# Optimization experiments

Measured on AMD Instinct MI355X. Metric: run time of the kernel, lower is better.

The kernel has to match this reference:

```python
import jax, jax.numpy as jnp
import numpy as np

N_STEPS = 2
S_MAX = 3.0
BUDGET = 32.0

def _unit(x):
    n = jnp.linalg.norm(x, axis=-1, keepdims=True)
    return x / jnp.maximum(n, 1e-12)

def setup_inputs() -> dict:
    key = jax.random.key(0)
    ks = jax.random.split(key, 12)
    BS, B, M, D, N = 8, 4, 2048, 128, 1024
    seed = jax.random.normal(ks[0], (BS, N, D), jnp.float32)
    w_cand = jax.random.normal(ks[1], (BS, N, D), jnp.float32)
    novelty = jax.random.uniform(ks[2], (BS, N), jnp.float32)
    g_em = jax.random.uniform(ks[3], (BS,), jnp.float32)
    em_K = _unit(jax.random.normal(ks[4], (BS, B, M, D), jnp.float32))
    em_V = jax.random.normal(ks[5], (BS, B, M, D), jnp.float32)
    em_S = jax.random.uniform(ks[6], (BS, B, M), jnp.float32)
    em_age = jax.random.uniform(ks[7], (BS, B, M), jnp.float32)
    w1 = jax.random.normal(ks[8], (B, D), jnp.float32) * 0.02
    w2 = jax.random.normal(ks[9], (B, D), jnp.float32) * 0.02
    gate_bias = jnp.zeros((B, D), jnp.float32)
    raw_tau = jnp.zeros((B,), jnp.float32)
    raw_tau_w = jnp.zeros((B,), jnp.float32)
    return dict(seed=seed, w_cand=w_cand, novelty=novelty, g_em=g_em,
                em_K=em_K, em_V=em_V, em_S=em_S, em_age=em_age,
                w1=w1, w2=w2, gate_bias=gate_bias,
                raw_tau=raw_tau, raw_tau_w=raw_tau_w, b=0)

def reference(seed, w_cand, novelty, g_em, em_K, em_V, em_S, em_age,
              w1, w2, gate_bias, raw_tau, raw_tau_w, b):
    Kb = em_K[:, b]          # [BS, M, D]
    Vb = em_V[:, b]          # [BS, M, D]
    Sb = em_S[:, b]          # [BS, M]
    ageb = em_age[:, b]      # [BS, M]
    active = (Sb > 0)[:, None, :]  # [BS, 1, M]

    # ---- trail_read (eval mode: no sigma noise) ----
    tau = jax.nn.softplus(raw_tau[b]) + 0.1
    y = seed
    for _ in range(N_STEPS):
        scores = jnp.einsum('bnd,bmd->bnm', y, Kb) / tau
        scores = jnp.where(active, scores, -jnp.inf)
        attn = jnp.nan_to_num(jax.nn.softmax(scores, axis=-1), nan=0.0)
        delta = jnp.einsum('bnm,bmd->bnd', attn, Vb)
        gate = jax.nn.sigmoid(w1[b] * y + w2[b] * delta + gate_bias[b])
        y = y + gate * delta
    y_em = y - seed

    # ---- commit: soft routing -> aggregate -> neuromodulated EMA ----
    tau_w = jax.nn.softplus(raw_tau_w[b]) + 0.1
    M_slots = Kb.shape[1]
    w_norm = _unit(w_cand)
    route_scores = jnp.einsum('bnd,bmd->bnm', w_norm, Kb) / tau_w
    route_scores = jnp.where(active, route_scores, -jnp.inf)
    route = jnp.nan_to_num(jax.nn.softmax(route_scores, axis=-1), nan=1.0 / M_slots)
    weighted_route = novelty[..., None] * route           # [BS, N, M]
    route_agg = weighted_route.mean(axis=1)               # [BS, M]
    denom = jnp.maximum(weighted_route.sum(axis=1), 1e-8)[..., None]  # [BS, M, 1]
    update_K = jnp.einsum('bnm,bnd->bmd', weighted_route, w_norm) / denom
    update_V = jnp.einsum('bnm,bnd->bmd', weighted_route, w_cand) / denom
    alpha = jnp.minimum(g_em[:, None] * route_agg, 1.0)   # [BS, M]
    a = alpha[..., None]
    new_K = (1 - a) * Kb + a * _unit(update_K)
    new_V = (1 - a) * Vb + a * update_V
    new_S = jnp.clip(Sb + alpha, 0.0, S_MAX)
    new_age = ageb * (1 - alpha)
    # budget_enforce: rescale strengths so each row sums to at most BUDGET
    scale = jnp.minimum(1.0, BUDGET / jnp.maximum(new_S.sum(-1, keepdims=True), 1e-8))
    new_S = new_S * scale
    return (y_em, new_K, new_V, new_S, new_age)
```

## Files before the change

kernel.cpp:

```cpp
#include <hip/hip_runtime.h>
#include <hip/hip_bf16.h>
#include <math.h>

#define BS_ 8
#define B_  4
#define M_  2048
#define D_  128
#define N_  1024
#define NEG (-1e30f)

typedef unsigned short us_t;
typedef __attribute__((ext_vector_type(8))) short bf8v;
typedef __attribute__((ext_vector_type(4))) float f4v;

__device__ __forceinline__ float softplus_(float x) {
    return (x > 20.0f) ? x : log1pf(expf(x));
}
__device__ __forceinline__ float dot4_acc(float4 a, float4 b, float acc) {
    acc = fmaf(a.x, b.x, acc);
    acc = fmaf(a.y, b.y, acc);
    acc = fmaf(a.z, b.z, acc);
    acc = fmaf(a.w, b.w, acc);
    return acc;
}
__device__ __forceinline__ us_t f2bf(float x) {
    __hip_bfloat16 h = __float2bfloat16(x);
    return __builtin_bit_cast(us_t, h);
}
__device__ __forceinline__ float bf2f(us_t u) {
    unsigned v = ((unsigned)u) << 16;
    return __builtin_bit_cast(float, v);
}
__device__ __forceinline__ int swz(int us_idx, int row) { return us_idx ^ ((row & 7) << 3); }

__global__ __launch_bounds__(256, 2) void conv_k(
    const float* __restrict__ w_cand, const float* __restrict__ emK,
    const float* __restrict__ emV, const int* __restrict__ bp,
    us_t* __restrict__ Kbf, us_t* __restrict__ Wcg,
    us_t* __restrict__ WcTg, us_t* __restrict__ Vtg, float* __restrict__ invnW)
{
    __shared__ float wt[64][132];
    __shared__ float invn[64];
    const int tid = threadIdx.x;
    const int bs  = blockIdx.y;
    const int bx  = blockIdx.x;
    const int b   = bp[0];

    if (bx < 32) {
        const float* src = emK + ((size_t)(bs * B_ + b)) * M_ * D_ + (size_t)bx * 64 * D_;
        us_t* dst = Kbf + (size_t)bs * M_ * D_ + (size_t)bx * 64 * D_;
        for (int i = tid; i < 64 * 128 / 4; i += 256) {
            float4 v = ((const float4*)src)[i];
            ushort4 o;
            o.x = f2bf(v.x); o.y = f2bf(v.y); o.z = f2bf(v.z); o.w = f2bf(v.w);
            ((ushort4*)dst)[i] = o;
        }
        return;
    }
    if (bx >= 48) {
        const int m0 = (bx - 48) * 64;
        const float* Vb = emV + ((size_t)(bs * B_ + b)) * M_ * D_ + (size_t)m0 * D_;
        for (int c = tid; c < 64 * 32; c += 256) {
            int row = c >> 5, col = (c & 31) << 2;
            *(float4*)&wt[row][col] = *(const float4*)&Vb[row * D_ + col];
        }
        __syncthreads();
        us_t* VtB = Vtg + (size_t)bs * D_ * M_;
        for (int c = tid; c < 1024; c += 256) {
            int d = c >> 3, mc = c & 7;
            uint4 o;
            o.x = (unsigned)f2bf(wt[mc * 8 + 0][d]) | ((unsigned)f2bf(wt[mc * 8 + 1][d]) << 16);
            o.y = (unsigned)f2bf(wt[mc * 8 + 2][d]) | ((unsigned)f2bf(wt[mc * 8 + 3][d]) << 16);
            o.z = (unsigned)f2bf(wt[mc * 8 + 4][d]) | ((unsigned)f2bf(wt[mc * 8 + 5][d]) << 16);
            o.w = (unsigned)f2bf(wt[mc * 8 + 6][d]) | ((unsigned)f2bf(wt[mc * 8 + 7][d]) << 16);
            *(uint4*)&VtB[(size_t)d * M_ + m0 + mc * 8] = o;
        }
        return;
    }
    const int n0 = (bx - 32) * 64;
    const float* Wb = w_cand + (size_t)bs * N_ * D_ + (size_t)n0 * D_;
    for (int c = tid; c < 64 * 32; c += 256) {
        int row = c >> 5, col = (c & 31) << 2;
        *(float4*)&wt[row][col] = *(const float4*)&Wb[row * D_ + col];
    }
    __syncthreads();
    {
        int r = tid >> 2, j = tid & 3;
        float ss = 0.0f;
        #pragma unroll
        for (int q = 0; q < 8; ++q) {
            float4 v = *(float4*)&wt[r][q * 16 + j * 4];
            ss = dot4_acc(v, v, ss);
        }
        ss += __shfl_xor(ss, 1, 4);
        ss += __shfl_xor(ss, 2, 4);
        if (j == 0) invn[r] = 1.0f / fmaxf(sqrtf(ss), 1e-12f);
    }
    __syncthreads();
    us_t* WcB = Wcg + (size_t)bs * N_ * D_ + (size_t)n0 * D_;
    for (int e = tid; e < 8192; e += 256) {
        int row = e >> 7, col = e & 127;
        WcB[row * D_ + col] = f2bf(wt[row][col]);
    }
    us_t* WcTB = WcTg + (size_t)bs * D_ * N_;
    for (int e = tid; e < 8192; e += 256) {
        int d = e >> 6, n = e & 63;
        WcTB[d * N_ + n0 + n] = f2bf(wt[n][d]);
    }
    if (tid < 64) invnW[(size_t)bs * N_ + n0 + tid] = invn[tid];
}

__global__ __launch_bounds__(256, 2) void attn_part_k(
    const float* __restrict__ ySrc, const us_t* __restrict__ Kbf,
    const us_t* __restrict__ Vtg, const float* __restrict__ emS,
    const float* __restrict__ raw_tau, const int* __restrict__ bp,
    us_t* __restrict__ pDelta, float2* __restrict__ pML)
{
    __shared__ us_t KtL[2][8192];
    __shared__ us_t VtL[2][8192];
    __shared__ us_t Pl[4][1024];
    __shared__ float sbt[2][64];

    const int tid = threadIdx.x;
    const int raw = blockIdx.x;
    const int logical = (raw & 7) * 64 + (raw >> 3);
    const int bs = logical >> 6;
    const int rem = logical & 63;
    const int nt = rem >> 2;
    const int q  = rem & 3;
    const int b = bp[0];
    const float rtau = 1.0f / (softplus_(raw_tau[b]) + 0.1f);

    const us_t* KbB = Kbf + (size_t)bs * M_ * D_ + (size_t)(q * 512) * D_;
    const us_t* VtB = Vtg + (size_t)bs * D_ * M_;
    const float* SbB = emS + ((size_t)(bs * B_ + b)) * M_ + q * 512;

    const int wave = tid >> 6, lane = tid & 63;
    const int r = lane & 15, kg = lane >> 4;

    bf8v yb[4];
    {
        const float* yrow = ySrc + ((size_t)bs * N_ + nt * 64 + wave * 16 + r) * D_;
        #pragma unroll
        for (int kk = 0; kk < 4; ++kk) {
            float4 a = *(const float4*)&yrow[kk * 32 + kg * 8];
            float4 c = *(const float4*)&yrow[kk * 32 + kg * 8 + 4];
            bf8v t;
            t[0] = (short)f2bf(a.x); t[1] = (short)f2bf(a.y);
            t[2] = (short)f2bf(a.z); t[3] = (short)f2bf(a.w);
            t[4] = (short)f2bf(c.x); t[5] = (short)f2bf(c.y);
            t[6] = (short)f2bf(c.z); t[7] = (short)f2bf(c.w);
            yb[kk] = t;
        }
    }

    uint4 kr[4], vr[4];
    float sreg = 0.0f;

#define AP_LOAD(t) do {                                                           \
        for (int i = 0; i < 4; ++i) {                                             \
            int c = tid + i * 256;                                                \
            kr[i] = *(const uint4*)&KbB[(size_t)((t) * 64 + (c >> 4)) * D_ + ((c & 15) << 3)]; \
            vr[i] = *(const uint4*)&VtB[(size_t)(c >> 3) * M_ + q * 512 + (t) * 64 + ((c & 7) << 3)]; \
        }                                                                         \
        if (tid < 64) sreg = SbB[(t) * 64 + tid];                                 \
    } while (0)

#define AP_WRITE(bf) do {                                                         \
        for (int i = 0; i < 4; ++i) {                                             \
            int c = tid + i * 256;                                                \
            int ki = (c >> 4) * 128 + ((c & 15) << 3);                            \
            *(uint4*)&KtL[bf][swz(ki, c >> 4)] = kr[i];                           \
            int vi = (c >> 3) * 64 + ((c & 7) << 3);                              \
            *(uint4*)&VtL[bf][swz(vi, c >> 3)] = vr[i];                           \
        }                                                                         \
        if (tid < 64) sbt[bf][tid] = sreg;                                        \
    } while (0)

    f4v cD[8];
    #pragma unroll
    for (int df = 0; df < 8; ++df) cD[df] = (f4v){0.f, 0.f, 0.f, 0.f};
    float mrun = NEG, lsum = 0.0f;

    AP_LOAD(0);
    AP_WRITE(0);
    __syncthreads();

    for (int t = 0; t < 8; ++t) {
        const int cur = t & 1;
        if (t < 7) AP_LOAD(t + 1);

        float sv[4][4];
        #pragma unroll
        for (int mf = 0; mf < 4; ++mf) {
            f4v c4 = {0.f, 0.f, 0.f, 0.f};
            #pragma unroll
            for (int kk = 0; kk < 4; ++kk) {
                int row_ = mf * 16 + r;
                bf8v a = *(bf8v*)&KtL[cur][swz(row_ * 128 + kk * 32 + kg * 8, row_)];
                c4 = __builtin_amdgcn_mfma_f32_16x16x32_bf16(a, yb[kk], c4, 0, 0, 0);
            }
            #pragma unroll
            for (int reg = 0; reg < 4; ++reg) {
                int ml = mf * 16 + kg * 4 + reg;
                sv[mf][reg] = (sbt[cur][ml] > 0.0f) ? c4[reg] * rtau : NEG;
            }
        }
        float tmax = NEG;
        #pragma unroll
        for (int mf = 0; mf < 4; ++mf)
            #pragma unroll
            for (int reg = 0; reg < 4; ++reg) tmax = fmaxf(tmax, sv[mf][reg]);
        tmax = fmaxf(tmax, __shfl_xor(tmax, 16, 64));
        tmax = fmaxf(tmax, __shfl_xor(tmax, 32, 64));
        float mnew = fmaxf(mrun, tmax);
        float f = (mnew > -1e29f) ? __expf(mrun - mnew) : 1.0f;
        mrun = mnew;

        float psum = 0.0f;
        #pragma unroll
        for (int mf = 0; mf < 4; ++mf)
            #pragma unroll
            for (int reg = 0; reg < 4; ++reg) {
                float p = (sv[mf][reg] > -1e29f) ? __expf(sv[mf][reg] - mnew) : 0.0f;
                psum += p;
                int ml = mf * 16 + kg * 4 + reg;
                Pl[wave][swz(r * 64 + ml, r)] = f2bf(p);
            }
        lsum = lsum * f + psum;

        float fr[4];
        #pragma unroll
        for (int reg = 0; reg < 4; ++reg) fr[reg] = __shfl(f, kg * 4 + reg, 64);
        #pragma unroll
        for (int df = 0; df < 8; ++df)
            #pragma unroll
            for (int reg = 0; reg < 4; ++reg) cD[df][reg] *= fr[reg];

        #pragma unroll
        for (int kk = 0; kk < 2; ++kk) {
            bf8v pa = *(bf8v*)&Pl[wave][swz(r * 64 + kk * 32 + kg * 8, r)];
            #pragma unroll
            for (int df = 0; df < 8; ++df) {
                int row_ = df * 16 + r;
                bf8v bv = *(bf8v*)&VtL[cur][swz(row_ * 64 + kk * 32 + kg * 8, row_)];
                cD[df] = __builtin_amdgcn_mfma_f32_16x16x32_bf16(pa, bv, cD[df], 0, 0, 0);
            }
        }

        if (t < 7) AP_WRITE(cur ^ 1);
        __syncthreads();
    }
#undef AP_LOAD
#undef AP_WRITE

    lsum += __shfl_xor(lsum, 16, 64);
    lsum += __shfl_xor(lsum, 32, 64);
    float invl = (lsum > 0.0f) ? 1.0f / lsum : 0.0f;

    us_t* pd = pDelta + ((size_t)((bs * 16 + nt) * 4 + q)) * (64 * 128);
    #pragma unroll
    for (int reg = 0; reg < 4; ++reg) {
        float il = __shfl(invl, kg * 4 + reg, 64);
        int nrow = wave * 16 + kg * 4 + reg;
        #pragma unroll
        for (int df = 0; df < 8; ++df)
            pd[nrow * 128 + df * 16 + r] = f2bf(cD[df][reg] * il);
    }
    if (kg == 0) {
        int nrow = wave * 16 + r;
        pML[((size_t)((bs * 16 + nt) * 4 + q)) * 64 + nrow] = make_float2(mrun, lsum);
    }
}

__global__ __launch_bounds__(256, 2) void attn_merge_k(
    const float* __restrict__ ySrc, const float* __restrict__ seed,
    const us_t* __restrict__ pDelta, const float2* __restrict__ pML,
    const float* __restrict__ w1, const float* __restrict__ w2,
    const float* __restrict__ gb, const int* __restrict__ bp,
    float* __restrict__ yOut, int mode)
{
    __shared__ float w1L[128], w2L[128], gbL[128];
    const int tid = threadIdx.x, raw = blockIdx.x;
    const int logical = (raw & 7) * 16 + (raw >> 3);
    const int bs = logical >> 4, nt = logical & 15;
    const int b = bp[0];
    if (tid < 128) {
        w1L[tid] = w1[b * D_ + tid];
        w2L[tid] = w2[b * D_ + tid];
        gbL[tid] = gb[b * D_ + tid];
    }
    __syncthreads();
    const int rw = tid >> 2, dj = tid & 3;
    const size_t base = ((size_t)(bs * 16 + nt)) * 4;
    float2 ml0 = pML[(base + 0) * 64 + rw];
    float2 ml1 = pML[(base + 1) * 64 + rw];
    float2 ml2 = pML[(base + 2) * 64 + rw];
    float2 ml3 = pML[(base + 3) * 64 + rw];
    float M = fmaxf(fmaxf(ml0.x, ml1.x), fmaxf(ml2.x, ml3.x));
    float w0 = 0.f, wA = 0.f, wB = 0.f, w3 = 0.f, tot = 0.f;
    if (M > -1e29f) {
        w0 = ml0.y * __expf(ml0.x - M);
        wA = ml1.y * __expf(ml1.x - M);
        wB = ml2.y * __expf(ml2.x - M);
        w3 = ml3.y * __expf(ml3.x - M);
        tot = w0 + wA + wB + w3;
    }
    float inv = (tot > 0.0f) ? 1.0f / tot : 0.0f;
    w0 *= inv; wA *= inv; wB *= inv; w3 *= inv;

    const us_t* pd0 = pDelta + (base + 0) * 8192 + rw * 128;
    const us_t* pd1 = pDelta + (base + 1) * 8192 + rw * 128;
    const us_t* pd2 = pDelta + (base + 2) * 8192 + rw * 128;
    const us_t* pd3 = pDelta + (base + 3) * 8192 + rw * 128;
    const float* yrow = ySrc + ((size_t)bs * N_ + nt * 64 + rw) * D_;
    const float* srow = seed + ((size_t)bs * N_ + nt * 64 + rw) * D_;
    float* orow = yOut + ((size_t)bs * N_ + nt * 64 + rw) * D_;

    #pragma unroll
    for (int e = 0; e < 4; ++e) {
        int d0 = dj * 32 + e * 8;
        uint4 u0 = *(const uint4*)&pd0[d0];
        uint4 u1 = *(const uint4*)&pd1[d0];
        uint4 u2 = *(const uint4*)&pd2[d0];
        uint4 u3 = *(const uint4*)&pd3[d0];
        const us_t* a0 = (const us_t*)&u0;
        const us_t* a1 = (const us_t*)&u1;
        const us_t* a2 = (const us_t*)&u2;
        const us_t* a3 = (const us_t*)&u3;
        float4 ya = *(const float4*)&yrow[d0];
        float4 yc = *(const float4*)&yrow[d0 + 4];
        float yv[8] = {ya.x, ya.y, ya.z, ya.w, yc.x, yc.y, yc.z, yc.w};
        float res[8];
        #pragma unroll
        for (int j = 0; j < 8; ++j) {
            float dl = w0 * bf2f(a0[j]) + wA * bf2f(a1[j]) + wB * bf2f(a2[j]) + w3 * bf2f(a3[j]);
            int d = d0 + j;
            float g = 1.0f / (1.0f + __expf(-(w1L[d] * yv[j] + w2L[d] * dl + gbL[d])));
            res[j] = yv[j] + g * dl;
        }
        if (mode == 1) {
            float4 sa = *(const float4*)&srow[d0];
            float4 sc = *(const float4*)&srow[d0 + 4];
            res[0] -= sa.x; res[1] -= sa.y; res[2] -= sa.z; res[3] -= sa.w;
            res[4] -= sc.x; res[5] -= sc.y; res[6] -= sc.z; res[7] -= sc.w;
        }
        float4 o1; o1.x = res[0]; o1.y = res[1]; o1.z = res[2]; o1.w = res[3];
        float4 o2; o2.x = res[4]; o2.y = res[5]; o2.z = res[6]; o2.w = res[7];
        *(float4*)&orow[d0] = o1;
        *(float4*)&orow[d0 + 4] = o2;
    }
}

__global__ __launch_bounds__(256, 2) void stats_k(
    const us_t* __restrict__ Wcg, const us_t* __restrict__ Kbf,
    const float* __restrict__ invnW, const float* __restrict__ emS,
    const float* __restrict__ raw_tau_w, const int* __restrict__ bp,
    float* __restrict__ mxW, float* __restrict__ smW)
{
    __shared__ us_t KtL[2][8192];
    __shared__ float sbt[2][64];

    const int tid = threadIdx.x;
    const int raw = blockIdx.x;
    const int logical = (raw & 7) * 64 + (raw >> 3);
    const int bs = logical >> 6;
    const int rem = logical & 63;
    const int nt = rem >> 2;
    const int q  = rem & 3;
    const int b = bp[0];
    const float rtw = 1.0f / (softplus_(raw_tau_w[b]) + 0.1f);

    const us_t* KbB = Kbf + (size_t)bs * M_ * D_ + (size_t)(q * 512) * D_;
    const float* SbB = emS + ((size_t)(bs * B_ + b)) * M_ + q * 512;

    const int wave = tid >> 6, lane = tid & 63;
    const int r = lane & 15, kg = lane >> 4;
    const int n = nt * 64 + wave * 16 + r;

    bf8v wb[4];
    {
        const us_t* wrow = Wcg + ((size_t)bs * N_ + n) * D_;
        #pragma unroll
        for (int kk = 0; kk < 4; ++kk)
            wb[kk] = *(const bf8v*)&wrow[kk * 32 + kg * 8];
    }
    const float ivn = invnW[(size_t)bs * N_ + n];

    uint4 kr[4];
    float sreg = 0.0f;

#define ST_LOAD(t) do {                                                           \
        for (int i = 0; i < 4; ++i) {                                             \
            int c = tid + i * 256;                                                \
            kr[i] = *(const uint4*)&KbB[(size_t)((t) * 64 + (c >> 4)) * D_ + ((c & 15) << 3)]; \
        }                                                                         \
        if (tid < 64) sreg = SbB[(t) * 64 + tid];                                 \
    } while (0)

#define ST_WRITE(bf) do {                                                         \
        for (int i = 0; i < 4; ++i) {                                             \
            int c = tid + i * 256;                                                \
            int ki = (c >> 4) * 128 + ((c & 15) << 3);                            \
            *(uint4*)&KtL[bf][swz(ki, c >> 4)] = kr[i];                           \
        }                                                                         \
        if (tid < 64) sbt[bf][tid] = sreg;                                        \
    } while (0)

    float mx = NEG, sm = 0.0f;

    ST_LOAD(0);
    ST_WRITE(0);
    __syncthreads();

    for (int t = 0; t < 8; ++t) {
        const int cur = t & 1;
        if (t < 7) ST_LOAD(t + 1);

        #pragma unroll
        for (int mf = 0; mf < 4; ++mf) {
            f4v c4 = {0.f, 0.f, 0.f, 0.f};
            #pragma unroll
            for (int kk = 0; kk < 4; ++kk) {
                int row_ = mf * 16 + r;
                bf8v a = *(bf8v*)&KtL[cur][swz(row_ * 128 + kk * 32 + kg * 8, row_)];
                c4 = __builtin_amdgcn_mfma_f32_16x16x32_bf16(a, wb[kk], c4, 0, 0, 0);
            }
            float v[4]; bool act[4];
            float lm = NEG;
            #pragma unroll
            for (int reg = 0; reg < 4; ++reg) {
                int ml = mf * 16 + kg * 4 + reg;
                v[reg] = c4[reg] * ivn * rtw;
                act[reg] = (sbt[cur][ml] > 0.0f);
                if (act[reg]) lm = fmaxf(lm, v[reg]);
            }
            float mnew = fmaxf(mx, lm);
            if (mnew > -1e29f) {
                float acc = sm * __expf(mx - mnew);
                #pragma unroll
                for (int reg = 0; reg < 4; ++reg)
                    if (act[reg]) acc += __expf(v[reg] - mnew);
                sm = acc; mx = mnew;
            }
        }

        if (t < 7) ST_WRITE(cur ^ 1);
        __syncthreads();
    }
#undef ST_LOAD
#undef ST_WRITE

    #pragma unroll
    for (int off = 16; off <= 32; off <<= 1) {
        float omx = __shfl_xor(mx, off, 64);
        float osm = __shfl_xor(sm, off, 64);
        float nm = fmaxf(mx, omx);
        if (nm > -1e29f) sm = sm * __expf(mx - nm) + osm * __expf(omx - nm);
        else sm = 0.0f;
        mx = nm;
    }
    if (kg == 0) {
        mxW[(size_t)(q * BS_ + bs) * N_ + n] = mx;
        smW[(size_t)(q * BS_ + bs) * N_ + n] = sm;
    }
}

__global__ __launch_bounds__(256) void stats_fin_k(
    const float* __restrict__ mxW, const float* __restrict__ smW,
    const float* __restrict__ novelty,
    float* __restrict__ mxF, float* __restrict__ rivF, float* __restrict__ punF)
{
    int idx = blockIdx.x * 256 + threadIdx.x;
    float m[4], s[4];
    #pragma unroll
    for (int q = 0; q < 4; ++q) {
        m[q] = mxW[q * (BS_ * N_) + idx];
        s[q] = smW[q * (BS_ * N_) + idx];
    }
    float MX = fmaxf(fmaxf(m[0], m[1]), fmaxf(m[2], m[3]));
    float SM = 0.0f;
    if (MX > -1e29f) {
        #pragma unroll
        for (int q = 0; q < 4; ++q)
            if (m[q] > -1e29f) SM += s[q] * __expf(m[q] - MX);
    }
    float nov = novelty[idx];
    if (SM > 0.0f) { mxF[idx] = MX; rivF[idx] = nov / SM; punF[idx] = -1.0f; }
    else           { mxF[idx] = 0.0f; rivF[idx] = 0.0f; punF[idx] = nov * (1.0f / (float)M_); }
}

__global__ __launch_bounds__(256) void update2_k(
    const us_t* __restrict__ Kbf, const us_t* __restrict__ Wcg,
    const us_t* __restrict__ WcTg, const float* __restrict__ g_em,
    const float* __restrict__ emK, const float* __restrict__ emV,
    const float* __restrict__ emS, const float* __restrict__ emAge,
    const float* __restrict__ raw_tau_w, const int* __restrict__ bp,
    const float* __restrict__ invnW, const float* __restrict__ mxF,
    const float* __restrict__ rivF, const float* __restrict__ punF,
    float* __restrict__ outK, float* __restrict__ outV,
    float* __restrict__ outS, float* __restrict__ outA)
{
    __shared__ us_t KaL[8192];
    __shared__ us_t WcL[2][8192];
    __shared__ us_t WcTL[2][8192];
    __shared__ us_t Pl[4096];
    __shared__ us_t P2l[4096];
    __shared__ float4 cns[2][64];
    __shared__ float sbL[64], csL[64], alphaL[64];

    const int tid = threadIdx.x;
    const int raw = blockIdx.x;
    const int logical = (raw & 7) * 32 + (raw >> 3);
    const int bs = logical >> 5;
    const int m0 = (logical & 31) * 64;
    const int b = bp[0];
    const float rtw = 1.0f / (softplus_(raw_tau_w[b]) + 0.1f);
    const float ge = g_em[bs];

    const us_t* KaG = Kbf + (size_t)bs * M_ * D_ + (size_t)m0 * D_;
    const us_t* WcB = Wcg + (size_t)bs * N_ * D_;
    const us_t* WcTB = WcTg + (size_t)bs * D_ * N_;

    for (int c = tid; c < 64 * 16; c += 256) {
        int row = c >> 4, off = (c & 15) << 3;
        uint4 v = *(const uint4*)&KaG[row * 128 + off];
        *(uint4*)&KaL[swz(row * 128 + off, row)] = v;
    }
    if (tid < 64) sbL[tid] = emS[((size_t)(bs * B_ + b)) * M_ + m0 + tid];
    __syncthreads();

    const int wave = tid >> 6, lane = tid & 63;
    const int r = lane & 15, kg = lane >> 4;
    const int mf = wave;

    bf8v a_s[4];
    #pragma unroll
    for (int kk = 0; kk < 4; ++kk) {
        int row = mf * 16 + r;
        a_s[kk] = *(bf8v*)&KaL[swz(row * 128 + kk * 32 + kg * 8, row)];
    }
    bool act4[4];
    #pragma unroll
    for (int reg = 0; reg < 4; ++reg) act4[reg] = (sbL[mf * 16 + kg * 4 + reg] > 0.0f);

    f4v cK[8], cV[8];
    #pragma unroll
    for (int df = 0; df < 8; ++df) { cK[df] = (f4v){0,0,0,0}; cV[df] = (f4v){0,0,0,0}; }
    float csp[4] = {0.f, 0.f, 0.f, 0.f};

    uint4 wr[4], wtr[4];
    float4 creg = {0.f, 0.f, 0.f, 0.f};

#define UP_LOAD(t) do {                                                            \
        for (int i = 0; i < 4; ++i) {                                              \
            int c = tid + i * 256;                                                 \
            wr[i]  = *(const uint4*)&WcB[((size_t)((t) * 64 + (c >> 4))) * D_ + ((c & 15) << 3)]; \
            wtr[i] = *(const uint4*)&WcTB[((size_t)(c >> 3)) * N_ + (t) * 64 + ((c & 7) << 3)];   \
        }                                                                          \
        if (tid < 64) {                                                            \
            int nn = (t) * 64 + tid;                                               \
            creg.x = mxF[(size_t)bs * N_ + nn];                                    \
            creg.y = rivF[(size_t)bs * N_ + nn];                                   \
            creg.z = punF[(size_t)bs * N_ + nn];                                   \
            creg.w = invnW[(size_t)bs * N_ + nn];                                  \
        }                                                                          \
    } while (0)

#define UP_WRITE(bf) do {                                                          \
        for (int i = 0; i < 4; ++i) {                                              \
            int c = tid + i * 256;                                                 \
            int ki = (c >> 4) * 128 + ((c & 15) << 3);                             \
            *(uint4*)&WcL[bf][swz(ki, c >> 4)] = wr[i];                            \
            int vi = (c >> 3) * 64 + ((c & 7) << 3);                               \
            *(uint4*)&WcTL[bf][swz(vi, c >> 3)] = wtr[i];                          \
        }                                                                          \
        if (tid < 64) cns[bf][tid] = creg;                                         \
    } while (0)

    UP_LOAD(0);
    UP_WRITE(0);
    __syncthreads();

    for (int nt = 0; nt < 16; ++nt) {
        const int cur = nt & 1;
        if (nt < 15) UP_LOAD(nt + 1);

        #pragma unroll
        for (int nf = 0; nf < 4; ++nf) {
            f4v c = {0.f, 0.f, 0.f, 0.f};
            #pragma unroll
            for (int kk = 0; kk < 4; ++kk) {
                int row = nf * 16 + r;
                bf8v bb = *(bf8v*)&WcL[cur][swz(row * 128 + kk * 32 + kg * 8, row)];
                c = __builtin_amdgcn_mfma_f32_16x16x32_bf16(a_s[kk], bb, c, 0, 0, 0);
            }
            int nl = nf * 16 + r;
            float4 cn = cns[cur][nl];
            #pragma unroll
            for (int reg = 0; reg < 4; ++reg) {
                float p;
                if (cn.z >= 0.0f) p = cn.z;
                else p = act4[reg] ? cn.y * __expf(c[reg] * cn.w * rtw - cn.x) : 0.0f;
                csp[reg] += p;
                int mrow = mf * 16 + kg * 4 + reg;
                Pl[swz(mrow * 64 + nl, mrow)] = f2bf(p);
                P2l[swz(mrow * 64 + nl, mrow)] = f2bf(p * cn.w);
            }
        }
        #pragma unroll
        for (int kk2 = 0; kk2 < 2; ++kk2) {
            int prow = mf * 16 + r;
            bf8v pa  = *(bf8v*)&Pl[swz(prow * 64 + kk2 * 32 + kg * 8, prow)];
            bf8v pa2 = *(bf8v*)&P2l[swz(prow * 64 + kk2 * 32 + kg * 8, prow)];
            #pragma unroll
            for (int df = 0; df < 8; ++df) {
                int row = df * 16 + r;
                bf8v bw = *(bf8v*)&WcTL[cur][swz(row * 64 + kk2 * 32 + kg * 8, row)];
                cV[df] = __builtin_amdgcn_mfma_f32_16x16x32_bf16(pa, bw, cV[df], 0, 0, 0);
                cK[df] = __builtin_amdgcn_mfma_f32_16x16x32_bf16(pa2, bw, cK[df], 0, 0, 0);
            }
        }

        if (nt < 15) UP_WRITE(cur ^ 1);
        __syncthreads();
    }
#undef UP_LOAD
#undef UP_WRITE

    #pragma unroll
    for (int reg = 0; reg < 4; ++reg) {
        float v = csp[reg];
        v += __shfl_xor(v, 1, 16);
        v += __shfl_xor(v, 2, 16);
        v += __shfl_xor(v, 4, 16);
        v += __shfl_xor(v, 8, 16);
        csp[reg] = v;
    }
    if (r == 0) {
        #pragma unroll
        for (int reg = 0; reg < 4; ++reg) csL[mf * 16 + kg * 4 + reg] = csp[reg];
    }
    __syncthreads();
    if (tid < 64) alphaL[tid] = fminf(ge * csL[tid] * (1.0f / (float)N_), 1.0f);
    __syncthreads();

    float rden[4], nrm[4];
    #pragma unroll
    for (int reg = 0; reg < 4; ++reg) {
        int ml = mf * 16 + kg * 4 + reg;
        rden[reg] = 1.0f / fmaxf(csL[ml], 1e-8f);
        float s = 0.0f;
        #pragma unroll
        for (int df = 0; df < 8; ++df) {
            float u = cK[df][reg] * rden[reg];
            s += u * u;
        }
        s += __shfl_xor(s, 1, 16);
        s += __shfl_xor(s, 2, 16);
        s += __shfl_xor(s, 4, 16);
        s += __shfl_xor(s, 8, 16);
        nrm[reg] = 1.0f / fmaxf(sqrtf(s), 1e-12f);
    }

    const float* KbG = emK + ((size_t)(bs * B_ + b)) * M_ * D_ + (size_t)m0 * D_;
    const float* VbG = emV + ((size_t)(bs * B_ + b)) * M_ * D_ + (size_t)m0 * D_;
    float* oK = outK + (size_t)bs * M_ * D_ + (size_t)m0 * D_;
    float* oV = outV + (size_t)bs * M_ * D_ + (size_t)m0 * D_;
    #pragma unroll
    for (int reg = 0; reg < 4; ++reg) {
        int ml = mf * 16 + kg * 4 + reg;
        float a = alphaL[ml];
        #pragma unroll
        for (int df = 0; df < 8; ++df) {
            int d = df * 16 + r;
            float uK = cK[df][reg] * rden[reg] * nrm[reg];
            float uV = cV[df][reg] * rden[reg];
            oK[ml * D_ + d] = (1.0f - a) * KbG[ml * D_ + d] + a * uK;
            oV[ml * D_ + d] = (1.0f - a) * VbG[ml * D_ + d] + a * uV;
        }
    }
    if (tid < 64) {
        float a = alphaL[tid];
        float sp = fminf(fmaxf(sbL[tid] + a, 0.0f), 3.0f);
        outS[(size_t)bs * M_ + m0 + tid] = sp;
        outA[(size_t)bs * M_ + m0 + tid] =
            emAge[((size_t)(bs * B_ + b)) * M_ + m0 + tid] * (1.0f - a);
    }
}

__global__ __launch_bounds__(256) void scale_s_k(float* __restrict__ outS)
{
    __shared__ float wsum[4];
    const int bs = blockIdx.x, tid = threadIdx.x;
    float* p = outS + (size_t)bs * M_;
    float s = 0.0f;
    for (int i = tid; i < M_; i += 256) s += p[i];
    #pragma unroll
    for (int o = 32; o >= 1; o >>= 1) s += __shfl_xor(s, o, 64);
    if ((tid & 63) == 0) wsum[tid >> 6] = s;
    __syncthreads();
    float tot = wsum[0] + wsum[1] + wsum[2] + wsum[3];
    float scale = fminf(1.0f, 32.0f / fmaxf(tot, 1e-8f));
    for (int i = tid; i < M_; i += 256) p[i] *= scale;
}

extern "C" void kernel_launch(void* const* d_in, const int* in_sizes, int n_in,
                              void* d_out, int out_size, void* d_ws, size_t ws_size,
                              hipStream_t stream) {
    (void)in_sizes; (void)n_in; (void)out_size; (void)ws_size;
    const float* seed    = (const float*)d_in[0];
    const float* w_cand  = (const float*)d_in[1];
    const float* novelty = (const float*)d_in[2];
    const float* g_em    = (const float*)d_in[3];
    const float* emK     = (const float*)d_in[4];
    const float* emV     = (const float*)d_in[5];
    const float* emS     = (const float*)d_in[6];
    const float* emAge   = (const float*)d_in[7];
    const float* w1      = (const float*)d_in[8];
    const float* w2      = (const float*)d_in[9];
    const float* gb      = (const float*)d_in[10];
    const float* rt      = (const float*)d_in[11];
    const float* rtw     = (const float*)d_in[12];
    const int*   bp      = (const int*)d_in[13];

    float* out  = (float*)d_out;
    float* yem  = out;
    float* outK = out + 1048576;
    float* outV = out + 3145728;
    float* outS = out + 5242880;
    float* outA = out + 5259264;

    us_t* Kbf = (us_t*)d_ws;
    us_t* Wcg = Kbf + (size_t)BS_ * M_ * D_;
    us_t* WcT = Wcg + (size_t)BS_ * N_ * D_;
    us_t* Vtg = WcT + (size_t)BS_ * D_ * N_;
    us_t* pDelta = Vtg + (size_t)BS_ * D_ * M_;
    float* fb   = (float*)(pDelta + (size_t)512 * 64 * 128);
    float* invnW = fb;
    float* mxW   = invnW + BS_ * N_;
    float* smW   = mxW + 4 * BS_ * N_;
    float* mxF   = smW + 4 * BS_ * N_;
    float* rivF  = mxF + BS_ * N_;
    float* punF  = rivF + BS_ * N_;
    float* y1    = punF + BS_ * N_;
    float2* pML  = (float2*)(y1 + (size_t)BS_ * N_ * D_);

    conv_k<<<dim3(80, 8), 256, 0, stream>>>(w_cand, emK, emV, bp, Kbf, Wcg, WcT, Vtg, invnW);

    attn_part_k<<<dim3(512), 256, 0, stream>>>(seed, Kbf, Vtg, emS, rt, bp, pDelta, pML);
    attn_merge_k<<<dim3(128), 256, 0, stream>>>(seed, seed, pDelta, pML, w1, w2, gb, bp, y1, 0);
    attn_part_k<<<dim3(512), 256, 0, stream>>>(y1, Kbf, Vtg, emS, rt, bp, pDelta, pML);
    attn_merge_k<<<dim3(128), 256, 0, stream>>>(y1, seed, pDelta, pML, w1, w2, gb, bp, yem, 1);

    stats_k<<<dim3(512), 256, 0, stream>>>(Wcg, Kbf, invnW, emS, rtw, bp, mxW, smW);
    stats_fin_k<<<dim3(32), 256, 0, stream>>>(mxW, smW, novelty, mxF, rivF, punF);
    update2_k<<<dim3(256), 256, 0, stream>>>(Kbf, Wcg, WcT, g_em, emK, emV, emS, emAge,
                                             rtw, bp, invnW, mxF, rivF, punF,
                                             outK, outV, outS, outA);
    scale_s_k<<<8, 256, 0, stream>>>(outS);
}
```

Baseline: 268.2 us.

## Split update kernel into 32-row tiles with N-split waves and LDS reduction

The commit update kernel now processes 32 memory slots per block instead of 64, launching 512 blocks instead of 256. Within each block, the four waves split as two M-fragments times two N-halves, and partial K/V accumulators are reduced through shared memory at the end. The double-buffered LDS staging is replaced by a single buffer with register prefetch, and the K fragments are loaded straight from global memory. This aims to raise occupancy and parallelism on the many-CU GPU, at the cost of extra syncs per tile, an extra reduction, and loading the same W tiles twice as often overall.

Result: slower. 294.1 us (+9.7%).

```diff
diff --git a/kernel.cpp b/kernel.cpp
--- a/kernel.cpp
+++ b/kernel.cpp
@@ -31,6 +31,7 @@
     unsigned v = ((unsigned)u) << 16;
     return __builtin_bit_cast(float, v);
 }
+__device__ __forceinline__ bf8v gfrag(const us_t* p) { return *(const bf8v*)p; }
 __device__ __forceinline__ int swz(int us_idx, int row) { return us_idx ^ ((row & 7) << 3); }
 
 __global__ __launch_bounds__(256, 2) void conv_k(
@@ -383,7 +384,7 @@
         const us_t* wrow = Wcg + ((size_t)bs * N_ + n) * D_;
         #pragma unroll
         for (int kk = 0; kk < 4; ++kk)
-            wb[kk] = *(const bf8v*)&wrow[kk * 32 + kg * 8];
+            wb[kk] = gfrag(&wrow[kk * 32 + kg * 8]);
     }
     const float ivn = invnW[(size_t)bs * N_ + n];
 
@@ -490,7 +491,7 @@
     else           { mxF[idx] = 0.0f; rivF[idx] = 0.0f; punF[idx] = nov * (1.0f / (float)M_); }
 }
 
-__global__ __launch_bounds__(256) void update2_k(
+__global__ __launch_bounds__(256) void update4_k(
     const us_t* __restrict__ Kbf, const us_t* __restrict__ Wcg,
     const us_t* __restrict__ WcTg, const float* __restrict__ g_em,
     const float* __restrict__ emK, const float* __restrict__ emV,
@@ -501,48 +502,42 @@
     float* __restrict__ outK, float* __restrict__ outV,
     float* __restrict__ outS, float* __restrict__ outA)
 {
-    __shared__ us_t KaL[8192];
-    __shared__ us_t WcL[2][8192];
-    __shared__ us_t WcTL[2][8192];
-    __shared__ us_t Pl[4096];
-    __shared__ us_t P2l[4096];
-    __shared__ float4 cns[2][64];
-    __shared__ float sbL[64], csL[64], alphaL[64];
+    __shared__ __align__(16) char smraw[32768];
+    us_t* WcS  = (us_t*)smraw;
+    us_t* WcTS = (us_t*)(smraw + 16384);
+    __shared__ us_t Pl[2][1024];
+    __shared__ us_t P2l[2][1024];
+    __shared__ float4 cns[64];
+    __shared__ float4 pcs[2][64];
 
     const int tid = threadIdx.x;
     const int raw = blockIdx.x;
-    const int logical = (raw & 7) * 32 + (raw >> 3);
-    const int bs = logical >> 5;
-    const int m0 = (logical & 31) * 64;
+    const int logical = (raw & 7) * 64 + (raw >> 3);
+    const int bs = logical >> 6;
+    const int m0 = (logical & 63) * 32;
     const int b = bp[0];
     const float rtw = 1.0f / (softplus_(raw_tau_w[b]) + 0.1f);
     const float ge = g_em[bs];
 
-    const us_t* KaG = Kbf + (size_t)bs * M_ * D_ + (size_t)m0 * D_;
-    const us_t* WcB = Wcg + (size_t)bs * N_ * D_;
+    const int wave = tid >> 6, lane = tid & 63;
+    const int mf = wave & 1, nfh = wave >> 1;
+    const int r = lane & 15, kg = lane >> 4;
+    const int mrow0 = m0 + mf * 16;
+
+    const us_t* WcB  = Wcg + (size_t)bs * N_ * D_;
     const us_t* WcTB = WcTg + (size_t)bs * D_ * N_;
-
-    for (int c = tid; c < 64 * 16; c += 256) {
-        int row = c >> 4, off = (c & 15) << 3;
-        uint4 v = *(const uint4*)&KaG[row * 128 + off];
-        *(uint4*)&KaL[swz(row * 128 + off, row)] = v;
-    }
-    if (tid < 64) sbL[tid] = emS[((size_t)(bs * B_ + b)) * M_ + m0 + tid];
-    __syncthreads();
-
-    const int wave = tid >> 6, lane = tid & 63;
-    const int r = lane & 15, kg = lane >> 4;
-    const int mf = wave;
+    const float* SbRow = emS + ((size_t)(bs * B_ + b)) * M_ + mrow0;
 
     bf8v a_s[4];
-    #pragma unroll
-    for (int kk = 0; kk < 4; ++kk) {
-        int row = mf * 16 + r;
-        a_s[kk] = *(bf8v*)&KaL[swz(row * 128 + kk * 32 + kg * 8, row)];
+    {
+        const us_t* arow = Kbf + ((size_t)bs * M_ + mrow0 + r) * D_;
+        #pragma unroll
+        for (int kk = 0; kk < 4; ++kk)
+            a_s[kk] = gfrag(&arow[kk * 32 + kg * 8]);
     }
     bool act4[4];
     #pragma unroll
-    for (int reg = 0; reg < 4; ++reg) act4[reg] = (sbL[mf * 16 + kg * 4 + reg] > 0.0f);
+    for (int reg = 0; reg < 4; ++reg) act4[reg] = (SbRow[kg * 4 + reg] > 0.0f);
 
     f4v cK[8], cV[8];
     #pragma unroll
@@ -552,7 +547,7 @@
     uint4 wr[4], wtr[4];
     float4 creg = {0.f, 0.f, 0.f, 0.f};
 
-#define UP_LOAD(t) do {                                                            \
+#define U4_LOAD(t) do {                                                            \
         for (int i = 0; i < 4; ++i) {                                              \
             int c = tid + i * 256;                                                 \
             wr[i]  = *(const uint4*)&WcB[((size_t)((t) * 64 + (c >> 4))) * D_ + ((c & 15) << 3)]; \
@@ -567,66 +562,90 @@
         }                                                                          \
     } while (0)
 
-#define UP_WRITE(bf) do {                                                          \
+#define U4_WRITE() do {                                                            \
         for (int i = 0; i < 4; ++i) {                                              \
             int c = tid + i * 256;                                                 \
             int ki = (c >> 4) * 128 + ((c & 15) << 3);                             \
-            *(uint4*)&WcL[bf][swz(ki, c >> 4)] = wr[i];                            \
+            *(uint4*)&WcS[swz(ki, c >> 4)] = wr[i];                                \
             int vi = (c >> 3) * 64 + ((c & 7) << 3);                               \
-            *(uint4*)&WcTL[bf][swz(vi, c >> 3)] = wtr[i];                          \
+            *(uint4*)&WcTS[swz(vi, c >> 3)] = wtr[i];                              \
         }                                                                          \
-        if (tid < 64) cns[bf][tid] = creg;                                         \
+        if (tid < 64) cns[tid] = creg;                                             \
     } while (0)
 
-    UP_LOAD(0);
-    UP_WRITE(0);
+    U4_LOAD(0);
+    U4_WRITE();
+    U4_LOAD(1);
     __syncthreads();
 
     for (int nt = 0; nt < 16; ++nt) {
-        const int cur = nt & 1;
-        if (nt < 15) UP_LOAD(nt + 1);
-
-        #pragma unroll
-        for (int nf = 0; nf < 4; ++nf) {
+        #pragma unroll
+        for (int nf2 = 0; nf2 < 2; ++nf2) {
+            const int nf = nfh * 2 + nf2;
             f4v c = {0.f, 0.f, 0.f, 0.f};
             #pragma unroll
             for (int kk = 0; kk < 4; ++kk) {
                 int row = nf * 16 + r;
-                bf8v bb = *(bf8v*)&WcL[cur][swz(row * 128 + kk * 32 + kg * 8, row)];
+                bf8v bb = *(bf8v*)&WcS[swz(row * 128 + kk * 32 + kg * 8, row)];
                 c = __builtin_amdgcn_mfma_f32_16x16x32_bf16(a_s[kk], bb, c, 0, 0, 0);
             }
             int nl = nf * 16 + r;
-            float4 cn = cns[cur][nl];
+            float4 cn = cns[nl];
             #pragma unroll
             for (int reg = 0; reg < 4; ++reg) {
                 float p;
                 if (cn.z >= 0.0f) p = cn.z;
                 else p = act4[reg] ? cn.y * __expf(c[reg] * cn.w * rtw - cn.x) : 0.0f;
                 csp[reg] += p;
-                int mrow = mf * 16 + kg * 4 + reg;
-                Pl[swz(mrow * 64 + nl, mrow)] = f2bf(p);
-                P2l[swz(mrow * 64 + nl, mrow)] = f2bf(p * cn.w);
-            }
-        }
-        #pragma unroll
-        for (int kk2 = 0; kk2 < 2; ++kk2) {
-            int prow = mf * 16 + r;
-            bf8v pa  = *(bf8v*)&Pl[swz(prow * 64 + kk2 * 32 + kg * 8, prow)];
-            bf8v pa2 = *(bf8v*)&P2l[swz(prow * 64 + kk2 * 32 + kg * 8, prow)];
+                int mr = kg * 4 + reg;
+                Pl[mf][swz(mr * 64 + nl, mr)] = f2bf(p);
+                P2l[mf][swz(mr * 64 + nl, mr)] = f2bf(p * cn.w);
+            }
+        }
+        {
+            bf8v pa  = *(bf8v*)&Pl[mf][swz(r * 64 + nfh * 32 + kg * 8, r)];
+            bf8v pa2 = *(bf8v*)&P2l[mf][swz(r * 64 + nfh * 32 + kg * 8, r)];
             #pragma unroll
             for (int df = 0; df < 8; ++df) {
                 int row = df * 16 + r;
-                bf8v bw = *(bf8v*)&WcTL[cur][swz(row * 64 + kk2 * 32 + kg * 8, row)];
+                bf8v bw = *(bf8v*)&WcTS[swz(row * 64 + nfh * 32 + kg * 8, row)];
                 cV[df] = __builtin_amdgcn_mfma_f32_16x16x32_bf16(pa, bw, cV[df], 0, 0, 0);
                 cK[df] = __builtin_amdgcn_mfma_f32_16x16x32_bf16(pa2, bw, cK[df], 0, 0, 0);
             }
         }
-
-        if (nt < 15) UP_WRITE(cur ^ 1);
-        __syncthreads();
-    }
-#undef UP_LOAD
-#undef UP_WRITE
+        if (nt < 15) {
+            __syncthreads();
+            U4_WRITE();
+            if (nt + 2 < 16) U4_LOAD(nt + 2);
+            __syncthreads();
+        }
+    }
+#undef U4_LOAD
+#undef U4_WRITE
+
+    __syncthreads();
+    f4v* pK = (f4v*)smraw;
+    f4v* pV = (f4v*)(smraw + 16384);
+    if (nfh == 1) {
+        #pragma unroll
+        for (int df = 0; df < 8; ++df) {
+            pK[(mf * 8 + df) * 64 + lane] = cK[df];
+            pV[(mf * 8 + df) * 64 + lane] = cV[df];
+        }
+        pcs[mf][lane] = make_float4(csp[0], csp[1], csp[2], csp[3]);
+    }
+    __syncthreads();
+    if (nfh == 1) return;
+
+    #pragma unroll
+    for (int df = 0; df < 8; ++df) {
+        cK[df] += pK[(mf * 8 + df) * 64 + lane];
+        cV[df] += pV[(mf * 8 + df) * 64 + lane];
+    }
+    {
+        float4 pc = pcs[mf][lane];
+        csp[0] += pc.x; csp[1] += pc.y; csp[2] += pc.z; csp[3] += pc.w;
+    }
 
     #pragma unroll
     for (int reg = 0; reg < 4; ++reg) {
@@ -637,19 +656,13 @@
         v += __shfl_xor(v, 8, 16);
         csp[reg] = v;
     }
-    if (r == 0) {
-        #pragma unroll
-        for (int reg = 0; reg < 4; ++reg) csL[mf * 16 + kg * 4 + reg] = csp[reg];
-    }
-    __syncthreads();
-    if (tid < 64) alphaL[tid] = fminf(ge * csL[tid] * (1.0f / (float)N_), 1.0f);
-    __syncthreads();
-
-    float rden[4], nrm[4];
+
+    float rden[4], nrm[4], alpha4[4];
     #pragma unroll
     for (int reg = 0; reg < 4; ++reg) {
-        int ml = mf * 16 + kg * 4 + reg;
-        rden[reg] = 1.0f / fmaxf(csL[ml], 1e-8f);
+        float csv = csp[reg];
+        alpha4[reg] = fminf(ge * csv * (1.0f / (float)N_), 1.0f);
+        rden[reg] = 1.0f / fmaxf(csv, 1e-8f);
         float s = 0.0f;
         #pragma unroll
         for (int df = 0; df < 8; ++df) {
@@ -663,29 +676,36 @@
         nrm[reg] = 1.0f / fmaxf(sqrtf(s), 1e-12f);
     }
 
-    const float* KbG = emK + ((size_t)(bs * B_ + b)) * M_ * D_ + (size_t)m0 * D_;
-    const float* VbG = emV + ((size_t)(bs * B_ + b)) * M_ * D_ + (size_t)m0 * D_;
-    float* oK = outK + (size_t)bs * M_ * D_ + (size_t)m0 * D_;
-    float* oV = outV + (size_t)bs * M_ * D_ + (size_t)m0 * D_;
+    const float* KbR = emK + ((size_t)(bs * B_ + b)) * M_ * D_ + (size_t)mrow0 * D_;
+    const float* VbR = emV + ((size_t)(bs * B_ + b)) * M_ * D_ + (size_t)mrow0 * D_;
+    float* oK = outK + (size_t)bs * M_ * D_ + (size_t)mrow0 * D_;
+    float* oV = outV + (size_t)bs * M_ * D_ + (size_t)mrow0 * D_;
     #pragma unroll
     for (int reg = 0; reg < 4; ++reg) {
-        int ml = mf * 16 + kg * 4 + reg;
-        float a = alphaL[ml];
+        int ml = kg * 4 + reg;
+        float a = alpha4[reg];
         #pragma unroll
         for (int df = 0; df < 8; ++df) {
             int d = df * 16 + r;
             float uK = cK[df][reg] * rden[reg] * nrm[reg];
             float uV = cV[df][reg] * rden[reg];
-            oK[ml * D_ + d] = (1.0f - a) * KbG[ml * D_ + d] + a * uK;
-            oV[ml * D_ + d] = (1.0f - a) * VbG[ml * D_ + d] + a * uV;
-        }
-    }
-    if (tid < 64) {
-        float a = alphaL[tid];
-        float sp = fminf(fmaxf(sbL[tid] + a, 0.0f), 3.0f);
-        outS[(size_t)bs * M_ + m0 + tid] = sp;
-        outA[(size_t)bs * M_ + m0 + tid] =
-            emAge[((size_t)(bs * B_ + b)) * M_ + m0 + tid] * (1.0f - a);
+            oK[ml * D_ + d] = (1.0f - a) * KbR[ml * D_ + d] + a * uK;
+            oV[ml * D_ + d] = (1.0f - a) * VbR[ml * D_ + d] + a * uV;
+        }
+    }
+    float cs0 = __shfl(csp[0], (r >> 2) * 16, 64);
+    float cs1 = __shfl(csp[1], (r >> 2) * 16, 64);
+    float cs2 = __shfl(csp[2], (r >> 2) * 16, 64);
+    float cs3 = __shfl(csp[3], (r >> 2) * 16, 64);
+    if (kg == 0) {
+        int sel = r & 3;
+        float csv = (sel == 0) ? cs0 : (sel == 1) ? cs1 : (sel == 2) ? cs2 : cs3;
+        float a = fminf(ge * csv * (1.0f / (float)N_), 1.0f);
+        float sb = SbRow[r];
+        float sp = fminf(fmaxf(sb + a, 0.0f), 3.0f);
+        outS[(size_t)bs * M_ + mrow0 + r] = sp;
+        outA[(size_t)bs * M_ + mrow0 + r] =
+            emAge[((size_t)(bs * B_ + b)) * M_ + mrow0 + r] * (1.0f - a);
     }
 }
 
@@ -736,7 +756,7 @@
     us_t* WcT = Wcg + (size_t)BS_ * N_ * D_;
     us_t* Vtg = WcT + (size_t)BS_ * D_ * N_;
     us_t* pDelta = Vtg + (size_t)BS_ * D_ * M_;
-    float* fb   = (float*)(pDelta + (size_t)512 * 64 * 128);
+    float* fb    = (float*)(pDelta + (size_t)512 * 64 * 128);
     float* invnW = fb;
     float* mxW   = invnW + BS_ * N_;
     float* smW   = mxW + 4 * BS_ * N_;
@@ -755,7 +775,7 @@
 
     stats_k<<<dim3(512), 256, 0, stream>>>(Wcg, Kbf, invnW, emS, rtw, bp, mxW, smW);
     stats_fin_k<<<dim3(32), 256, 0, stream>>>(mxW, smW, novelty, mxF, rivF, punF);
-    update2_k<<<dim3(256), 256, 0, stream>>>(Kbf, Wcg, WcT, g_em, emK, emV, emS, emAge,
+    update4_k<<<dim3(512), 256, 0, stream>>>(Kbf, Wcg, WcT, g_em, emK, emV, emS, emAge,
                                              rtw, bp, invnW, mxF, rivF, punF,
                                              outK, outV, outS, outA);
     scale_s_k<<<8, 256, 0, stream>>>(outS);
```
